# Optimization experiments

Measured on AMD Instinct MI355X. Metric: run time of the kernel, lower is better.

Reference implementation:

```python
import jax, jax.numpy as jnp
import numpy as np

N_NODES = 50000
N_EDGES = 800000
NODE_IN = 16
EDGE_IN = 3
G_DIM = 8
LATENT = 128
NODE_OUT = 1
EDGE_OUT = 1


def _dense_init(key, fan_in, fan_out):
    # flax default: lecun_normal weights, zero bias
    w = jax.random.normal(key, (fan_in, fan_out), jnp.float32) / jnp.sqrt(float(fan_in))
    b = jnp.zeros((fan_out,), jnp.float32)
    return w, b


def setup_inputs() -> dict:
    key = jax.random.key(0)
    ks = jax.random.split(key, 12)
    nodes = jax.random.normal(ks[0], (N_NODES, NODE_IN), jnp.float32)
    edges = jax.random.normal(ks[1], (N_EDGES, EDGE_IN), jnp.float32)
    globals_ = jax.random.normal(ks[2], (1, G_DIM), jnp.float32)
    senders = jax.random.randint(ks[3], (N_EDGES,), 0, N_NODES, jnp.int32)
    receivers = jax.random.randint(ks[4], (N_EDGES,), 0, N_NODES, jnp.int32)
    W_en, b_en = _dense_init(ks[5], NODE_IN, LATENT)      # encoder node Dense
    W_ee, b_ee = _dense_init(ks[6], EDGE_IN, LATENT)      # encoder edge Dense
    mlp_in = 3 * LATENT + G_DIM                           # concat(nodes, sent, recv, globals)
    W1, b1 = _dense_init(ks[7], mlp_in, LATENT)           # node MLP layer 1 (relu)
    W2, b2 = _dense_init(ks[8], LATENT, LATENT)           # node MLP layer 2
    W_dn, b_dn = _dense_init(ks[9], LATENT, NODE_OUT)     # decoder node Dense
    W_de, b_de = _dense_init(ks[10], LATENT, EDGE_OUT)    # decoder edge Dense
    return dict(nodes=nodes, edges=edges, globals_=globals_, senders=senders,
                receivers=receivers, W_en=W_en, b_en=b_en, W_ee=W_ee, b_ee=b_ee,
                W1=W1, b1=b1, W2=W2, b2=b2, W_dn=W_dn, b_dn=b_dn, W_de=W_de, b_de=b_de)


def reference(nodes, edges, globals_, senders, receivers,
              W_en, b_en, W_ee, b_ee, W1, b1, W2, b2, W_dn, b_dn, W_de, b_de):
    n = nodes.shape[0]
    # Encoder (GraphMapFeatures)
    h_n = nodes @ W_en + b_en                     # [N, L]
    h_e = edges @ W_ee + b_ee                     # [E, L]
    # One jraph.GraphNetwork step, update_edge_fn=None -> edges unchanged.
    # sent/received aggregation = segment_sum of edge features by sender/receiver.
    sent = jax.ops.segment_sum(h_e, senders, num_segments=n)      # [N, L]
    recv = jax.ops.segment_sum(h_e, receivers, num_segments=n)    # [N, L]
    gbc = jnp.broadcast_to(globals_[0], (n, globals_.shape[1]))   # single graph
    x = jnp.concatenate((h_n, sent, recv, gbc), axis=1)           # [N, 3L+G]
    x = jax.nn.relu(x @ W1 + b1)
    h_n = x @ W2 + b2
    # update_global_fn reconstructs concat([time], static) == globals (identity).
    # Decoder
    nodes_out = h_n @ W_dn + b_dn                 # [N, 1]
    edges_out = h_e @ W_de + b_de                 # [E, 1]
    return nodes_out, edges_out
```

## Files before the change

### kernel.cpp

```cpp
#include <hip/hip_runtime.h>

#define N_NODES 50000
#define N_EDGES 800000

#define CONSTS_OFF 0
#define SCAL_OFF   4096
#define GCNT_OFF   4160
#define REC_OFF    8192
#define CAP        40000
#define NBIN1      25
#define BINSZ      2000
#define NSUB       10
#define PARTS_OFF  (REC_OFF + 50 * CAP * 4)
#define PARTR_OFF  (PARTS_OFF + NSUB * N_NODES * 4)
#define WS_NEEDED  (PARTR_OFF + NSUB * N_NODES * 4)

__global__ void precompute_kernel(
    const float* __restrict__ g,
    const float* __restrict__ W_en,
    const float* __restrict__ b_en,
    const float* __restrict__ W_ee,
    const float* __restrict__ b_ee,
    const float* __restrict__ W1,
    const float* __restrict__ b1,
    const float* __restrict__ W2,
    const float* __restrict__ b2,
    const float* __restrict__ W_dn,
    const float* __restrict__ b_dn,
    const float* __restrict__ W_de,
    const float* __restrict__ b_de,
    float* __restrict__ ws)
{
    const int s = blockIdx.x;
    const int k = threadIdx.x;
    float* consts = ws + CONSTS_OFF;
    float* scal   = ws + SCAL_OFF;

    if (s < 16) {
        float acc = 0.f;
        for (int l = 0; l < 128; ++l)
            acc += W_en[s * 128 + l] * W1[l * 128 + k];
        consts[k * 32 + s] = acc;
    } else if (s < 19) {
        const int j = s - 16;
        float acc = 0.f;
        for (int l = 0; l < 128; ++l)
            acc += W_ee[j * 128 + l] * W1[(128 + l) * 128 + k];
        consts[k * 32 + s] = acc;
    } else if (s < 22) {
        const int j = s - 19;
        float acc = 0.f;
        for (int l = 0; l < 128; ++l)
            acc += W_ee[j * 128 + l] * W1[(256 + l) * 128 + k];
        consts[k * 32 + s] = acc;
    } else if (s == 22) {
        float acc = b1[k];
        for (int l = 0; l < 128; ++l)
            acc += b_en[l] * W1[l * 128 + k];
        for (int j = 0; j < 8; ++j)
            acc += g[j] * W1[(384 + j) * 128 + k];
        consts[k * 32 + 22] = acc;
    } else if (s == 23) {
        float acc = 0.f;
        for (int l = 0; l < 128; ++l)
            acc += b_ee[l] * W1[(128 + l) * 128 + k];
        consts[k * 32 + 23] = acc;
    } else if (s == 24) {
        float acc = 0.f;
        for (int l = 0; l < 128; ++l)
            acc += b_ee[l] * W1[(256 + l) * 128 + k];
        consts[k * 32 + 24] = acc;
    } else if (s == 25) {
        float acc = 0.f;
        for (int j = 0; j < 128; ++j)
            acc += W2[k * 128 + j] * W_dn[j];
        consts[k * 32 + 25] = acc;
        consts[k * 32 + 26] = 0.f;
        consts[k * 32 + 27] = 0.f;
    } else {
        if (k == 0) {
            float c = b_dn[0];
            for (int j = 0; j < 128; ++j) c += b2[j] * W_dn[j];
            scal[0] = c;
            float ce = b_de[0];
            for (int l = 0; l < 128; ++l) ce += b_ee[l] * W_de[l];
            scal[1] = ce;
            scal[5] = 0.f; scal[6] = 0.f; scal[7] = 0.f;
        }
        if (k < 3) {
            float acc = 0.f;
            for (int l = 0; l < 128; ++l)
                acc += W_ee[k * 128 + l] * W_de[l];
            scal[2 + k] = acc;
        }
    }
}

__device__ __forceinline__ void emit_rec(
    float4* __restrict__ rec, int* __restrict__ lbase, int* __restrict__ cur,
    int binside, int local, float x, float y, float z)
{
    int slot = lbase[binside] + atomicAdd(&cur[binside], 1);
    if (slot >= CAP) slot = CAP - 1;
    rec[(size_t)binside * CAP + slot] = make_float4(x, y, z, __int_as_float(local));
}

__global__ __launch_bounds__(256) void bucket_kernel(
    const float* __restrict__ edges,
    const int*   __restrict__ senders,
    const int*   __restrict__ receivers,
    const float* __restrict__ ws_ro,
    int*   __restrict__ gcnt,
    float4* __restrict__ rec,
    float* __restrict__ out_edges)
{
    __shared__ int hist[64], lbase[64], cur[64];
    const int tid = threadIdx.x;
    if (tid < 64) { hist[tid] = 0; cur[tid] = 0; }
    __syncthreads();

    const int e4 = (blockIdx.x * 256 + tid) * 4;
    const bool act = e4 < N_EDGES;

    int4 s4 = make_int4(0, 0, 0, 0), r4 = s4;
    unsigned bs0 = 0, bs1 = 0, bs2 = 0, bs3 = 0, br0 = 0, br1 = 0, br2 = 0, br3 = 0;
    if (act) {
        s4 = *(const int4*)(senders + e4);
        r4 = *(const int4*)(receivers + e4);
        bs0 = (unsigned)s4.x / BINSZ; bs1 = (unsigned)s4.y / BINSZ;
        bs2 = (unsigned)s4.z / BINSZ; bs3 = (unsigned)s4.w / BINSZ;
        br0 = (unsigned)r4.x / BINSZ; br1 = (unsigned)r4.y / BINSZ;
        br2 = (unsigned)r4.z / BINSZ; br3 = (unsigned)r4.w / BINSZ;
        atomicAdd(&hist[bs0], 1); atomicAdd(&hist[bs1], 1);
        atomicAdd(&hist[bs2], 1); atomicAdd(&hist[bs3], 1);
        atomicAdd(&hist[NBIN1 + br0], 1); atomicAdd(&hist[NBIN1 + br1], 1);
        atomicAdd(&hist[NBIN1 + br2], 1); atomicAdd(&hist[NBIN1 + br3], 1);
    }
    __syncthreads();
    if (tid < 2 * NBIN1)
        lbase[tid] = atomicAdd(&gcnt[tid], hist[tid]);
    __syncthreads();

    if (act) {
        const float4* ep = (const float4*)(edges + (size_t)e4 * 3);
        const float4 f0 = ep[0], f1 = ep[1], f2 = ep[2];
        const float* scal = ws_ro + SCAL_OFF;
        const float w0 = scal[2], w1 = scal[3], w2 = scal[4], cb = scal[1];
        float4 o;
        o.x = fmaf(f0.x, w0, fmaf(f0.y, w1, fmaf(f0.z, w2, cb)));
        o.y = fmaf(f0.w, w0, fmaf(f1.x, w1, fmaf(f1.y, w2, cb)));
        o.z = fmaf(f1.z, w0, fmaf(f1.w, w1, fmaf(f2.x, w2, cb)));
        o.w = fmaf(f2.y, w0, fmaf(f2.z, w1, fmaf(f2.w, w2, cb)));
        *(float4*)(out_edges + e4) = o;
        emit_rec(rec, lbase, cur, bs0,         s4.x - bs0 * BINSZ, f0.x, f0.y, f0.z);
        emit_rec(rec, lbase, cur, bs1,         s4.y - bs1 * BINSZ, f0.w, f1.x, f1.y);
        emit_rec(rec, lbase, cur, bs2,         s4.z - bs2 * BINSZ, f1.z, f1.w, f2.x);
        emit_rec(rec, lbase, cur, bs3,         s4.w - bs3 * BINSZ, f2.y, f2.z, f2.w);
        emit_rec(rec, lbase, cur, NBIN1 + br0, r4.x - br0 * BINSZ, f0.x, f0.y, f0.z);
        emit_rec(rec, lbase, cur, NBIN1 + br1, r4.y - br1 * BINSZ, f0.w, f1.x, f1.y);
        emit_rec(rec, lbase, cur, NBIN1 + br2, r4.z - br2 * BINSZ, f1.z, f1.w, f2.x);
        emit_rec(rec, lbase, cur, NBIN1 + br3, r4.w - br3 * BINSZ, f2.y, f2.z, f2.w);
    }
}

__global__ __launch_bounds__(512) void accum_kernel(
    const int* __restrict__ gcnt,
    const float4* __restrict__ rec,
    float* __restrict__ part_s,
    float* __restrict__ part_r)
{
    __shared__ float4 acc4[BINSZ];
    float* acc = (float*)acc4;
    const int tid = threadIdx.x;
    for (int i = tid; i < BINSZ; i += 512)
        acc4[i] = make_float4(0.f, 0.f, 0.f, 0.f);
    __syncthreads();

    const int sub = blockIdx.x;
    const int binside = blockIdx.y;
    int cnt = gcnt[binside];
    if (cnt > CAP) cnt = CAP;
    const int beg = (int)((long)sub * cnt / NSUB);
    const int end = (int)((long)(sub + 1) * cnt / NSUB);
    const float4* r = rec + (size_t)binside * CAP;

    for (int i = beg + tid; i < end; i += 512) {
        const float4 rc = r[i];
        const int li = __float_as_int(rc.w);
        atomicAdd(&acc[li * 4 + 0], rc.x);
        atomicAdd(&acc[li * 4 + 1], rc.y);
        atomicAdd(&acc[li * 4 + 2], rc.z);
        atomicAdd(&acc[li * 4 + 3], 1.0f);
    }
    __syncthreads();

    float* base = (binside < NBIN1 ? part_s : part_r)
                + (size_t)sub * (N_NODES * 4)
                + (size_t)(binside % NBIN1) * BINSZ * 4;
    float4* dst = (float4*)base;
    for (int i = tid; i < BINSZ; i += 512)
        dst[i] = acc4[i];
}

__global__ __launch_bounds__(256) void edge_kernel_atomic(
    const float* __restrict__ edges,
    const int*   __restrict__ senders,
    const int*   __restrict__ receivers,
    float* __restrict__ esr,
    const float* __restrict__ ws_ro,
    float* __restrict__ out_edges)
{
    const int e = blockIdx.x * 256 + threadIdx.x;
    if (e >= N_EDGES) return;
    const float e0 = edges[e * 3 + 0];
    const float e1 = edges[e * 3 + 1];
    const float e2 = edges[e * 3 + 2];
    const int s = senders[e];
    const int r = receivers[e];
    atomicAdd(&esr[s * 8 + 0], e0);
    atomicAdd(&esr[s * 8 + 1], e1);
    atomicAdd(&esr[s * 8 + 2], e2);
    atomicAdd(&esr[s * 8 + 3], 1.0f);
    atomicAdd(&esr[r * 8 + 4], e0);
    atomicAdd(&esr[r * 8 + 5], e1);
    atomicAdd(&esr[r * 8 + 6], e2);
    atomicAdd(&esr[r * 8 + 7], 1.0f);
    const float* scal = ws_ro + SCAL_OFF;
    out_edges[e] = e0 * scal[2] + e1 * scal[3] + e2 * scal[4] + scal[1];
}

__global__ __launch_bounds__(256) void node_kernel(
    const float* __restrict__ nodes,
    const float* __restrict__ ws,
    const float* __restrict__ part_s,
    const float* __restrict__ part_r,
    float* __restrict__ out_nodes,
    int use_parts)
{
    __shared__ float4 lds4[128 * 8];
    const float4* consts4 = (const float4*)(ws + CONSTS_OFF);
    for (int i = threadIdx.x; i < 128 * 8; i += 256)
        lds4[i] = consts4[i];
    __syncthreads();

    const int n = blockIdx.x * 256 + threadIdx.x;
    if (n >= N_NODES) return;

    const float4* np4 = (const float4*)(nodes + (size_t)n * 16);
    const float4 n0 = np4[0], n1 = np4[1], n2 = np4[2], n3 = np4[3];

    float4 es = make_float4(0.f, 0.f, 0.f, 0.f);
    float4 er = make_float4(0.f, 0.f, 0.f, 0.f);
    if (use_parts) {
#pragma unroll
        for (int c = 0; c < NSUB; ++c) {
            const float4 a = *(const float4*)(part_s + (size_t)c * (N_NODES * 4) + (size_t)n * 4);
            const float4 b = *(const float4*)(part_r + (size_t)c * (N_NODES * 4) + (size_t)n * 4);
            es.x += a.x; es.y += a.y; es.z += a.z; es.w += a.w;
            er.x += b.x; er.y += b.y; er.z += b.z; er.w += b.w;
        }
    } else {
        const float4* p = (const float4*)(ws + REC_OFF + (size_t)n * 8);
        es = p[0];
        er = p[1];
    }

    float acc = 0.f;
#pragma unroll 4
    for (int k = 0; k < 128; ++k) {
        const float4* c4 = &lds4[k * 8];
        const float4 m0 = c4[0], m1 = c4[1], m2 = c4[2], m3 = c4[3];
        const float4 q0 = c4[4];
        const float4 q1 = c4[5];
        const float4 q2 = c4[6];
        float pre = q1.z
            + n0.x * m0.x + n0.y * m0.y + n0.z * m0.z + n0.w * m0.w
            + n1.x * m1.x + n1.y * m1.y + n1.z * m1.z + n1.w * m1.w
            + n2.x * m2.x + n2.y * m2.y + n2.z * m2.z + n2.w * m2.w
            + n3.x * m3.x + n3.y * m3.y + n3.z * m3.z + n3.w * m3.w
            + es.x * q0.x + es.y * q0.y + es.z * q0.z
            + er.x * q0.w + er.y * q1.x + er.z * q1.y
            + es.w * q1.w + er.w * q2.x;
        acc += fmaxf(pre, 0.f) * q2.y;
    }
    const float* scal = ws + SCAL_OFF;
    out_nodes[n] = acc + scal[0];
}

extern "C" void kernel_launch(void* const* d_in, const int* in_sizes, int n_in,
                              void* d_out, int out_size, void* d_ws, size_t ws_size,
                              hipStream_t stream) {
    const float* nodes     = (const float*)d_in[0];
    const float* edges     = (const float*)d_in[1];
    const float* globals_  = (const float*)d_in[2];
    const int*   senders   = (const int*)d_in[3];
    const int*   receivers = (const int*)d_in[4];
    const float* W_en = (const float*)d_in[5];
    const float* b_en = (const float*)d_in[6];
    const float* W_ee = (const float*)d_in[7];
    const float* b_ee = (const float*)d_in[8];
    const float* W1   = (const float*)d_in[9];
    const float* b1   = (const float*)d_in[10];
    const float* W2   = (const float*)d_in[11];
    const float* b2   = (const float*)d_in[12];
    const float* W_dn = (const float*)d_in[13];
    const float* b_dn = (const float*)d_in[14];
    const float* W_de = (const float*)d_in[15];
    const float* b_de = (const float*)d_in[16];

    float* ws = (float*)d_ws;
    float* out = (float*)d_out;

    precompute_kernel<<<27, 128, 0, stream>>>(
        globals_, W_en, b_en, W_ee, b_ee, W1, b1, W2, b2,
        W_dn, b_dn, W_de, b_de, ws);

    const long ws_floats = (long)(ws_size / 4);
    const bool big = ws_floats >= (long)WS_NEEDED;

    int*    gcnt   = (int*)(ws + GCNT_OFF);
    float4* rec    = (float4*)(ws + REC_OFF);
    float*  part_s = ws + PARTS_OFF;
    float*  part_r = ws + PARTR_OFF;

    if (big) {
        hipMemsetAsync(gcnt, 0, 64 * sizeof(int), stream);
        bucket_kernel<<<(N_EDGES / 4 + 255) / 256, 256, 0, stream>>>(
            edges, senders, receivers, ws, gcnt, rec, out + N_NODES);
        dim3 grid(NSUB, 2 * NBIN1);
        accum_kernel<<<grid, 512, 0, stream>>>(gcnt, rec, part_s, part_r);
    } else {
        hipMemsetAsync(ws + REC_OFF, 0, (size_t)N_NODES * 8 * sizeof(float), stream);
        edge_kernel_atomic<<<(N_EDGES + 255) / 256, 256, 0, stream>>>(
            edges, senders, receivers, ws + REC_OFF, ws, out + N_NODES);
    }

    node_kernel<<<(N_NODES + 255) / 256, 256, 0, stream>>>(
        nodes, ws, part_s, part_r, out, big ? 1 : 0);
}
```

Measured before the change: 179.2 us.

## Use finer node bins so each accumulator block owns a whole segment

Bins shrink from 2000 to 500 nodes, which gives 200 segments. Each segment is reduced by a single 1024-thread block that writes final per-node sums straight to contiguous es/er arrays. This removes the 10-way partial buffers and their summation in the node kernel. Zeroing the counters moves into the precompute kernel, which drops a memset. In exchange each segment is processed serially by one block, the bucket kernel keeps more per-block histogram bins, and bucket writes scatter across more segments.

```diff
diff --git a/kernel.cpp b/kernel.cpp
--- a/kernel.cpp
+++ b/kernel.cpp
@@ -5,15 +5,15 @@
 
 #define CONSTS_OFF 0
 #define SCAL_OFF   4096
-#define GCNT_OFF   4160
-#define REC_OFF    8192
-#define CAP        40000
-#define NBIN1      25
-#define BINSZ      2000
-#define NSUB       10
-#define PARTS_OFF  (REC_OFF + 50 * CAP * 4)
-#define PARTR_OFF  (PARTS_OFF + NSUB * N_NODES * 4)
-#define WS_NEEDED  (PARTR_OFF + NSUB * N_NODES * 4)
+#define GCNT_OFF   4352
+#define ESRS_OFF   8192
+#define ESRR_OFF   208192
+#define REC_OFF    408192
+#define NBIN1      100
+#define BINSZ      500
+#define NSEG       200
+#define CAP        10000
+#define WS_NEEDED  (REC_OFF + NSEG * CAP * 4)
 
 __global__ void precompute_kernel(
     const float* __restrict__ g,
@@ -78,6 +78,9 @@
         consts[k * 32 + 26] = 0.f;
         consts[k * 32 + 27] = 0.f;
     } else {
+        int* gcnt = (int*)(ws + GCNT_OFF);
+        gcnt[k] = 0;
+        gcnt[128 + k] = 0;
         if (k == 0) {
             float c = b_dn[0];
             for (int j = 0; j < 128; ++j) c += b2[j] * W_dn[j];
@@ -97,12 +100,12 @@
 }
 
 __device__ __forceinline__ void emit_rec(
-    float4* __restrict__ rec, int* __restrict__ lbase, int* __restrict__ cur,
-    int binside, int local, float x, float y, float z)
-{
-    int slot = lbase[binside] + atomicAdd(&cur[binside], 1);
+    float4* __restrict__ rec, const int* __restrict__ lbase, int* __restrict__ cur,
+    int seg, int local, float x, float y, float z)
+{
+    int slot = lbase[seg] + atomicAdd(&cur[seg], 1);
     if (slot >= CAP) slot = CAP - 1;
-    rec[(size_t)binside * CAP + slot] = make_float4(x, y, z, __int_as_float(local));
+    rec[(size_t)seg * CAP + slot] = make_float4(x, y, z, __int_as_float(local));
 }
 
 __global__ __launch_bounds__(256) void bucket_kernel(
@@ -114,9 +117,9 @@
     float4* __restrict__ rec,
     float* __restrict__ out_edges)
 {
-    __shared__ int hist[64], lbase[64], cur[64];
+    __shared__ int hist[NSEG], lbase[NSEG], cur[NSEG];
     const int tid = threadIdx.x;
-    if (tid < 64) { hist[tid] = 0; cur[tid] = 0; }
+    for (int i = tid; i < NSEG; i += 256) { hist[i] = 0; cur[i] = 0; }
     __syncthreads();
 
     const int e4 = (blockIdx.x * 256 + tid) * 4;
@@ -137,8 +140,8 @@
         atomicAdd(&hist[NBIN1 + br2], 1); atomicAdd(&hist[NBIN1 + br3], 1);
     }
     __syncthreads();
-    if (tid < 2 * NBIN1)
-        lbase[tid] = atomicAdd(&gcnt[tid], hist[tid]);
+    for (int i = tid; i < NSEG; i += 256)
+        lbase[i] = atomicAdd(&gcnt[i], hist[i]);
     __syncthreads();
 
     if (act) {
@@ -163,28 +166,25 @@
     }
 }
 
-__global__ __launch_bounds__(512) void accum_kernel(
+__global__ __launch_bounds__(1024) void accum_kernel(
     const int* __restrict__ gcnt,
     const float4* __restrict__ rec,
-    float* __restrict__ part_s,
-    float* __restrict__ part_r)
+    float* __restrict__ es,
+    float* __restrict__ er)
 {
     __shared__ float4 acc4[BINSZ];
     float* acc = (float*)acc4;
     const int tid = threadIdx.x;
-    for (int i = tid; i < BINSZ; i += 512)
-        acc4[i] = make_float4(0.f, 0.f, 0.f, 0.f);
-    __syncthreads();
-
-    const int sub = blockIdx.x;
-    const int binside = blockIdx.y;
-    int cnt = gcnt[binside];
+    if (tid < BINSZ)
+        acc4[tid] = make_float4(0.f, 0.f, 0.f, 0.f);
+    __syncthreads();
+
+    const int seg = blockIdx.x;
+    int cnt = gcnt[seg];
     if (cnt > CAP) cnt = CAP;
-    const int beg = (int)((long)sub * cnt / NSUB);
-    const int end = (int)((long)(sub + 1) * cnt / NSUB);
-    const float4* r = rec + (size_t)binside * CAP;
-
-    for (int i = beg + tid; i < end; i += 512) {
+    const float4* r = rec + (size_t)seg * CAP;
+
+    for (int i = tid; i < cnt; i += 1024) {
         const float4 rc = r[i];
         const int li = __float_as_int(rc.w);
         atomicAdd(&acc[li * 4 + 0], rc.x);
@@ -194,19 +194,20 @@
     }
     __syncthreads();
 
-    float* base = (binside < NBIN1 ? part_s : part_r)
-                + (size_t)sub * (N_NODES * 4)
-                + (size_t)(binside % NBIN1) * BINSZ * 4;
+    float* base = (seg < NBIN1)
+                ? es + (size_t)seg * BINSZ * 4
+                : er + (size_t)(seg - NBIN1) * BINSZ * 4;
     float4* dst = (float4*)base;
-    for (int i = tid; i < BINSZ; i += 512)
-        dst[i] = acc4[i];
+    if (tid < BINSZ)
+        dst[tid] = acc4[tid];
 }
 
 __global__ __launch_bounds__(256) void edge_kernel_atomic(
     const float* __restrict__ edges,
     const int*   __restrict__ senders,
     const int*   __restrict__ receivers,
-    float* __restrict__ esr,
+    float* __restrict__ es,
+    float* __restrict__ er,
     const float* __restrict__ ws_ro,
     float* __restrict__ out_edges)
 {
@@ -217,14 +218,14 @@
     const float e2 = edges[e * 3 + 2];
     const int s = senders[e];
     const int r = receivers[e];
-    atomicAdd(&esr[s * 8 + 0], e0);
-    atomicAdd(&esr[s * 8 + 1], e1);
-    atomicAdd(&esr[s * 8 + 2], e2);
-    atomicAdd(&esr[s * 8 + 3], 1.0f);
-    atomicAdd(&esr[r * 8 + 4], e0);
-    atomicAdd(&esr[r * 8 + 5], e1);
-    atomicAdd(&esr[r * 8 + 6], e2);
-    atomicAdd(&esr[r * 8 + 7], 1.0f);
+    atomicAdd(&es[s * 4 + 0], e0);
+    atomicAdd(&es[s * 4 + 1], e1);
+    atomicAdd(&es[s * 4 + 2], e2);
+    atomicAdd(&es[s * 4 + 3], 1.0f);
+    atomicAdd(&er[r * 4 + 0], e0);
+    atomicAdd(&er[r * 4 + 1], e1);
+    atomicAdd(&er[r * 4 + 2], e2);
+    atomicAdd(&er[r * 4 + 3], 1.0f);
     const float* scal = ws_ro + SCAL_OFF;
     out_edges[e] = e0 * scal[2] + e1 * scal[3] + e2 * scal[4] + scal[1];
 }
@@ -232,10 +233,7 @@
 __global__ __launch_bounds__(256) void node_kernel(
     const float* __restrict__ nodes,
     const float* __restrict__ ws,
-    const float* __restrict__ part_s,
-    const float* __restrict__ part_r,
-    float* __restrict__ out_nodes,
-    int use_parts)
+    float* __restrict__ out_nodes)
 {
     __shared__ float4 lds4[128 * 8];
     const float4* consts4 = (const float4*)(ws + CONSTS_OFF);
@@ -248,22 +246,8 @@
 
     const float4* np4 = (const float4*)(nodes + (size_t)n * 16);
     const float4 n0 = np4[0], n1 = np4[1], n2 = np4[2], n3 = np4[3];
-
-    float4 es = make_float4(0.f, 0.f, 0.f, 0.f);
-    float4 er = make_float4(0.f, 0.f, 0.f, 0.f);
-    if (use_parts) {
-#pragma unroll
-        for (int c = 0; c < NSUB; ++c) {
-            const float4 a = *(const float4*)(part_s + (size_t)c * (N_NODES * 4) + (size_t)n * 4);
-            const float4 b = *(const float4*)(part_r + (size_t)c * (N_NODES * 4) + (size_t)n * 4);
-            es.x += a.x; es.y += a.y; es.z += a.z; es.w += a.w;
-            er.x += b.x; er.y += b.y; er.z += b.z; er.w += b.w;
-        }
-    } else {
-        const float4* p = (const float4*)(ws + REC_OFF + (size_t)n * 8);
-        es = p[0];
-        er = p[1];
-    }
+    const float4 es = *(const float4*)(ws + ESRS_OFF + (size_t)n * 4);
+    const float4 er = *(const float4*)(ws + ESRR_OFF + (size_t)n * 4);
 
     float acc = 0.f;
 #pragma unroll 4
@@ -318,23 +302,20 @@
     const long ws_floats = (long)(ws_size / 4);
     const bool big = ws_floats >= (long)WS_NEEDED;
 
-    int*    gcnt   = (int*)(ws + GCNT_OFF);
-    float4* rec    = (float4*)(ws + REC_OFF);
-    float*  part_s = ws + PARTS_OFF;
-    float*  part_r = ws + PARTR_OFF;
+    int*    gcnt = (int*)(ws + GCNT_OFF);
+    float4* rec  = (float4*)(ws + REC_OFF);
+    float*  es   = ws + ESRS_OFF;
+    float*  er   = ws + ESRR_OFF;
 
     if (big) {
-        hipMemsetAsync(gcnt, 0, 64 * sizeof(int), stream);
         bucket_kernel<<<(N_EDGES / 4 + 255) / 256, 256, 0, stream>>>(
             edges, senders, receivers, ws, gcnt, rec, out + N_NODES);
-        dim3 grid(NSUB, 2 * NBIN1);
-        accum_kernel<<<grid, 512, 0, stream>>>(gcnt, rec, part_s, part_r);
+        accum_kernel<<<NSEG, 1024, 0, stream>>>(gcnt, rec, es, er);
     } else {
-        hipMemsetAsync(ws + REC_OFF, 0, (size_t)N_NODES * 8 * sizeof(float), stream);
+        hipMemsetAsync(es, 0, (size_t)N_NODES * 8 * sizeof(float), stream);
         edge_kernel_atomic<<<(N_EDGES + 255) / 256, 256, 0, stream>>>(
-            edges, senders, receivers, ws + REC_OFF, ws, out + N_NODES);
-    }
-
-    node_kernel<<<(N_NODES + 255) / 256, 256, 0, stream>>>(
-        nodes, ws, part_s, part_r, out, big ? 1 : 0);
-}
+            edges, senders, receivers, es, er, ws, out + N_NODES);
+    }
+
+    node_kernel<<<(N_NODES + 255) / 256, 256, 0, stream>>>(nodes, ws, out);
+}
```

Measured after the change: 186.8 us. 4.2% more time.
